# Optimization experiments

Hardware: AMD Instinct MI355X
Metric: run time of the kernel (lower is better)

## Reference

```python
import jax, jax.numpy as jnp
import numpy as np


def _conv1x1(x, w):
    # x [N,I,D,H,W], w [O,I]
    return jnp.einsum('nidhw,oi->nodhw', x, w)


def _conv3x3(x, w):
    return jax.lax.conv_general_dilated(
        x, w, window_strides=(1, 1, 1), padding=[(1, 1)] * 3,
        dimension_numbers=('NCDHW', 'OIDHW', 'NCDHW'))


def _interp_axis(x, out_len, axis):
    # linear interpolation along one axis, align_corners=True
    in_len = x.shape[axis]
    scale = (in_len - 1) / (out_len - 1)
    pos = jnp.arange(out_len, dtype=x.dtype) * scale
    lo = jnp.clip(jnp.floor(pos).astype(jnp.int32), 0, in_len - 1)
    hi = jnp.minimum(lo + 1, in_len - 1)
    frac = pos - lo.astype(x.dtype)
    shp = [1] * x.ndim
    shp[axis] = out_len
    frac = frac.reshape(shp)
    return jnp.take(x, lo, axis=axis) * (1 - frac) + jnp.take(x, hi, axis=axis) * frac


def _upsample_trilinear_ac(x, size):
    for ax, s in zip((2, 3, 4), size):
        x = _interp_axis(x, s, ax)
    return x


def _grid_sample_3d(inp, grid):
    # inp [N,C,D,H,W]; grid [N,Do,Ho,Wo,3] with channels (x=w, y=h, z=d) in [-1,1]
    # matches torch grid_sample defaults: trilinear, align_corners=False, zeros padding
    N, C, D, H, W = inp.shape
    ix = ((grid[..., 0] + 1) * W - 1) * 0.5
    iy = ((grid[..., 1] + 1) * H - 1) * 0.5
    iz = ((grid[..., 2] + 1) * D - 1) * 0.5
    x0 = jnp.floor(ix).astype(jnp.int32)
    y0 = jnp.floor(iy).astype(jnp.int32)
    z0 = jnp.floor(iz).astype(jnp.int32)
    fx = ix - x0.astype(inp.dtype)
    fy = iy - y0.astype(inp.dtype)
    fz = iz - z0.astype(inp.dtype)
    flat = inp.reshape(N, C, D * H * W)
    out = jnp.zeros((N, C) + grid.shape[1:4], dtype=inp.dtype)
    for dz, wz in ((0, 1 - fz), (1, fz)):
        for dy, wy in ((0, 1 - fy), (1, fy)):
            for dx, wx in ((0, 1 - fx), (1, fx)):
                zc = z0 + dz
                yc = y0 + dy
                xc = x0 + dx
                valid = (zc >= 0) & (zc < D) & (yc >= 0) & (yc < H) & (xc >= 0) & (xc < W)
                idx = (jnp.clip(zc, 0, D - 1) * H + jnp.clip(yc, 0, H - 1)) * W + jnp.clip(xc, 0, W - 1)
                vals = jax.vmap(lambda f, i: f[:, i])(flat, idx)  # [N,C,Do,Ho,Wo]
                w = (wz * wy * wx) * valid.astype(inp.dtype)
                out = out + vals * w[:, None]
    return out


def _point_reinforce(x, w_atten, w_conv):
    # SE-style: global avg pool -> 1x1 conv -> sigmoid -> residual scale -> 1x1 conv
    pooled = jnp.mean(x, axis=(2, 3, 4), keepdims=True)
    atten = jax.nn.sigmoid(_conv1x1(pooled, w_atten))
    x = x + x * atten
    return _conv1x1(x, w_conv)


def _forward(x, y, w_down_h, w_down_l, w_flow, w_att_atten, w_att_conv):
    D, H, W = x.shape[2:]
    low = _conv1x1(x, w_down_l)
    low = _point_reinforce(low, w_att_atten, w_att_conv)
    hf = _conv1x1(y, w_down_h)
    hf = _upsample_trilinear_ac(hf, (D, H, W))
    flow = _conv3x3(jnp.concatenate([hf, low], axis=1), w_flow)  # [N,3,D,H,W]
    # coordinate grid, channel order (w, h, d) as in the original flow_warp
    gw = jnp.broadcast_to(jnp.arange(W, dtype=x.dtype)[None, None, :], (D, H, W))
    gh = jnp.broadcast_to(jnp.arange(H, dtype=x.dtype)[None, :, None], (D, H, W))
    gd = jnp.broadcast_to(jnp.arange(D, dtype=x.dtype)[:, None, None], (D, H, W))
    grid = jnp.stack([gw, gh, gd], axis=0)[None]  # [1,3,D,H,W]
    norm = jnp.array([W, H, D], dtype=x.dtype)
    # NOTE: faithful to original -- divides by size only (grid ends up in [0,1), not [-1,1])
    vgrid = jnp.transpose(grid + flow, (0, 2, 3, 4, 1)) / norm  # [N,D,H,W,3]
    return _grid_sample_3d(y, vgrid)


def setup_inputs() -> dict:
    key = jax.random.key(0)
    ks = jax.random.split(key, 7)
    inplane_l, inplane_h, outplane = 64, 128, 64
    x = jax.random.normal(ks[0], (2, inplane_l, 16, 64, 64), dtype=jnp.float32)
    y = jax.random.normal(ks[1], (2, inplane_h, 8, 32, 32), dtype=jnp.float32)
    s = 0.05
    w_down_h = jax.random.normal(ks[2], (outplane, inplane_h), dtype=jnp.float32) * s
    w_down_l = jax.random.normal(ks[3], (outplane, inplane_l), dtype=jnp.float32) * s
    w_flow = jax.random.normal(ks[4], (3, 2 * outplane, 3, 3, 3), dtype=jnp.float32) * s
    w_att_atten = jax.random.normal(ks[5], (inplane_l, inplane_l), dtype=jnp.float32) * s
    w_att_conv = jax.random.normal(ks[6], (inplane_l, inplane_l), dtype=jnp.float32) * s
    return {'x': x, 'y': y, 'w_down_h': w_down_h, 'w_down_l': w_down_l,
            'w_flow': w_flow, 'w_att_atten': w_att_atten, 'w_att_conv': w_att_conv}


def reference(x, y, w_down_h, w_down_l, w_flow, w_att_atten, w_att_conv):
    return _forward(x, y, w_down_h, w_down_l, w_flow, w_att_atten, w_att_conv)
```

## Files before the change

### kernel.cpp

```cpp
#include <hip/hip_runtime.h>
#include <math.h>


#define MEANX_OFF  0
#define WEFF_OFF   128
#define HF_OFF     16384
#define HFUP_OFF   1064960
#define VG_OFF     9453568
#define ZPAGE_OFF  9846784

__global__ __launch_bounds__(256) void kearly(const float* __restrict__ x,
                                              const float* __restrict__ y,
                                              const float* __restrict__ wdh,
                                              float* __restrict__ meanx,
                                              float* __restrict__ hf,
                                              float* __restrict__ zpage) {
    const int blk = blockIdx.x;
    if (blk < 128) {
        if (blk == 0 && threadIdx.x < 64) zpage[threadIdx.x] = 0.f;
        int ch = blk;
        const float4* base = (const float4*)(x + (size_t)ch * 65536);
        float s = 0.f;
        for (int j = threadIdx.x; j < 16384; j += 256) {
            float4 v = base[j];
            s += v.x + v.y + v.z + v.w;
        }
        __shared__ float red[256];
        red[threadIdx.x] = s;
        __syncthreads();
        for (int off = 128; off > 0; off >>= 1) {
            if (threadIdx.x < off) red[threadIdx.x] += red[threadIdx.x + off];
            __syncthreads();
        }
        if (threadIdx.x == 0) meanx[ch] = red[0] * (1.0f / 65536.0f);
    } else {
        const int b = blk - 128;
        const int n = b >> 7;
        const int r = b & 127;
        const int os = r & 3;
        const int tile = r >> 2;
        const int p = tile * 256 + threadIdx.x;
        const float* yb = y + (size_t)n * 128 * 8192 + p;

        float acc[16];
#pragma unroll
        for (int o = 0; o < 16; ++o) acc[o] = 0.f;

        for (int i = 0; i < 128; i += 4) {
            const float yi0 = yb[(size_t)(i + 0) * 8192];
            const float yi1 = yb[(size_t)(i + 1) * 8192];
            const float yi2 = yb[(size_t)(i + 2) * 8192];
            const float yi3 = yb[(size_t)(i + 3) * 8192];
#pragma unroll
            for (int o = 0; o < 16; ++o) {
                float a = acc[o];
                a = fmaf(wdh[(os * 16 + o) * 128 + i + 0], yi0, a);
                a = fmaf(wdh[(os * 16 + o) * 128 + i + 1], yi1, a);
                a = fmaf(wdh[(os * 16 + o) * 128 + i + 2], yi2, a);
                a = fmaf(wdh[(os * 16 + o) * 128 + i + 3], yi3, a);
                acc[o] = a;
            }
        }
        float* ob = hf + (size_t)(n * 64 + os * 16) * 8192 + p;
#pragma unroll
        for (int o = 0; o < 16; ++o)
            ob[(size_t)o * 8192] = acc[o];
    }
}

__global__ __launch_bounds__(256) void kprep(const float* __restrict__ wdl,
                                             const float* __restrict__ watt,
                                             const float* __restrict__ wconv,
                                             const float* __restrict__ wflow,
                                             const float* __restrict__ meanx,
                                             float* __restrict__ weff) {
    const int n = blockIdx.x;
    const int tid = threadIdx.x;
    __shared__ float s_wdl[4096];
    __shared__ float s_wcT[4096];
    __shared__ float s_flow[5184];
    __shared__ float pooled[64], sc[64];
    for (int k = tid; k < 4096; k += 256) {
        s_wdl[k] = wdl[k];
        int o = k >> 6, j = k & 63;
        s_wcT[j * 64 + o] = wconv[k];
    }
    for (int k = tid; k < 5184; k += 256) {
        int o = k / 1728, r = k - o * 1728;
        s_flow[k] = wflow[o * 3456 + 1728 + r];
    }
    __syncthreads();
    if (tid < 64) {
        float p = 0.f;
        for (int i = 0; i < 64; ++i) p += s_wdl[tid * 64 + i] * meanx[n * 64 + i];
        pooled[tid] = p;
    }
    __syncthreads();
    if (tid < 64) {
        float a = 0.f;
        for (int i = 0; i < 64; ++i) a += watt[tid * 64 + i] * pooled[i];
        sc[tid] = 1.f + 1.f / (1.f + expf(-a));
    }
    __syncthreads();
    float wc[16];
#pragma unroll
    for (int k = 0; k < 16; ++k) {
        const int idx = tid + 256 * k;
        const int o = idx & 63, i = idx >> 6;
        float acc = 0.f;
#pragma unroll 8
        for (int j = 0; j < 64; ++j)
            acc += s_wcT[j * 64 + o] * (sc[j] * s_wdl[j * 64 + i]);
        wc[k] = acc;
    }
    __syncthreads();
#pragma unroll
    for (int k = 0; k < 16; ++k) {
        const int idx = tid + 256 * k;
        const int o = idx & 63, i = idx >> 6;
        s_wdl[i * 64 + o] = wc[k];
    }
    __syncthreads();
    for (int e = tid; e < 5184; e += 256) {
        const int i = e / 81, r = e - i * 81;
        const int o = r / 27, tap = r - o * 27;
        float acc = 0.f;
#pragma unroll 8
        for (int c = 0; c < 64; ++c)
            acc += s_flow[o * 1728 + c * 27 + tap] * s_wdl[i * 64 + c];
        weff[n * 5184 + e] = acc;
    }
}

__global__ __launch_bounds__(256) void kmid(const float* __restrict__ x,
                                            const float* __restrict__ ws,
                                            const float* __restrict__ weff,
                                            const float* __restrict__ hf,
                                            float* __restrict__ hfup,
                                            float* __restrict__ part) {
    const int blk = blockIdx.x;
    if (blk < 1024) {
        const int tid = threadIdx.x;
        const int sp = blk & 7;
        const int tile = blk >> 3;
        const int n = tile >> 6;
        const int t = tile & 63;
        const int td = t >> 4, th = (t >> 2) & 3, tw = t & 3;
        const int d0 = td * 4, h0 = th * 16, w0 = tw * 16;
        const int xo = tid & 3, ty = (tid >> 2) & 15, tz = tid >> 6;
        const int wv = tid >> 6;

        __shared__ float lds[3][2048];

        const float* gb = x + (size_t)(n * 64 + sp * 8) * 65536;
        const float* zp = ws + ZPAGE_OFF;

        const float* addrk[8];
        int vmask = 0;
#pragma unroll
        for (int k = 0; k < 8; ++k) {
            const int e = tid + 256 * k;
            const int r = e / 18;
            const int lx = e - r * 18;
            const int z = r / 18;
            const int ly = r - z * 18;
            const int gz = d0 - 1 + z, gy = h0 - 1 + ly, gx = w0 - 1 + lx;
            const bool ok = (e < 1944) && ((unsigned)gz < 16u) && ((unsigned)gy < 64u) &&
                            ((unsigned)gx < 64u);
            addrk[k] = ok ? (gb + (gz * 4096 + gy * 64 + gx)) : zp;
            vmask |= (ok ? 1 : 0) << k;
        }

#define STAGEL(BUFI)                                                                  \
    {                                                                                 \
        _Pragma("unroll")                                                             \
        for (int k = 0; k < 8; ++k) {                                                 \
            __builtin_amdgcn_global_load_lds(                                         \
                (const __attribute__((address_space(1))) unsigned int*)(addrk[k]),    \
                (__attribute__((address_space(3))) unsigned int*)                     \
                    (&lds[BUFI][wv * 64 + 256 * k]),                                  \
                4, 0, 0);                                                             \
            addrk[k] += ((vmask >> k) & 1) ? 65536 : 0;                               \
        }                                                                             \
    }

        float acc[3][4];
#pragma unroll
        for (int o = 0; o < 3; ++o)
#pragma unroll
            for (int j = 0; j < 4; ++j) acc[o][j] = 0.f;

        STAGEL(0);

        for (int ci = 0; ci < 8; ++ci) {
            const int cur = ci % 3;
            if (ci < 7) {
                STAGEL((ci + 1) % 3);
                asm volatile("s_waitcnt vmcnt(8)" ::: "memory");
            } else {
                asm volatile("s_waitcnt vmcnt(0)" ::: "memory");
            }
            __builtin_amdgcn_s_barrier();
            __builtin_amdgcn_sched_barrier(0);

            const int cidx = __builtin_amdgcn_readfirstlane(sp * 8 + ci);
            const float* wbase = weff + (size_t)n * 5184 + (size_t)cidx * 81;
            const float* buf = lds[cur];
#pragma unroll
            for (int dz = 0; dz < 3; ++dz) {
#pragma unroll
                for (int dy = 0; dy < 3; ++dy) {
                    const float* rp = &buf[((tz + dz) * 18 + ty + dy) * 18 + 4 * xo];
                    const float2 a0 = *(const float2*)(rp);
                    const float2 a1 = *(const float2*)(rp + 2);
                    const float2 a2 = *(const float2*)(rp + 4);
                    const float v[6] = {a0.x, a0.y, a1.x, a1.y, a2.x, a2.y};
                    float wq[3][3];
#pragma unroll
                    for (int o = 0; o < 3; ++o)
#pragma unroll
                        for (int dx = 0; dx < 3; ++dx)
                            wq[o][dx] = wbase[o * 27 + (dz * 3 + dy) * 3 + dx];
#pragma unroll
                    for (int o = 0; o < 3; ++o)
#pragma unroll
                        for (int j = 0; j < 4; ++j)
#pragma unroll
                            for (int dx = 0; dx < 3; ++dx)
                                acc[o][j] = fmaf(wq[o][dx], v[j + dx], acc[o][j]);
                }
            }
        }
#undef STAGEL

        const int oz = d0 + tz, oy = h0 + ty, ox = w0 + 4 * xo;
        const size_t base = ((size_t)((sp + 8) * 2 + n)) * 3 * 65536;
        const int p = oz * 4096 + oy * 64 + ox;
#pragma unroll
        for (int o = 0; o < 3; ++o)
            *(float4*)(part + base + (size_t)o * 65536 + p) =
                make_float4(acc[o][0], acc[o][1], acc[o][2], acc[o][3]);
    } else {
        int id2 = (blk - 1024) * 256 + threadIdx.x;
        int wp = id2 & 31, h = (id2 >> 5) & 63, d = (id2 >> 11) & 15;
        int c = (id2 >> 15) & 63, n = id2 >> 21;
        const float SD = 7.0f / 15.0f, SH = 31.0f / 63.0f;
        float pd = (float)d * SD, ph = (float)h * SH;
        int z0 = (int)pd; if (z0 > 7) z0 = 7;
        int z1 = min(z0 + 1, 7); float fz = pd - (float)z0;
        int y0 = (int)ph; if (y0 > 31) y0 = 31;
        int y1 = min(y0 + 1, 31); float fy = ph - (float)y0;

        const int w0i = 2 * wp, w1i = 2 * wp + 1;
        float pw0 = (float)w0i * SH, pw1 = (float)w1i * SH;
        int xa = (int)pw0; if (xa > 31) xa = 31;
        float fx0 = pw0 - (float)xa;
        int xb2 = (int)pw1; if (xb2 > 31) xb2 = 31;
        float fx1 = pw1 - (float)xb2;

        const float* b = hf + (size_t)(n * 64 + c) * 8192;
        const int r00 = (z0 * 32 + y0) * 32, r01 = (z0 * 32 + y1) * 32;
        const int r10 = (z1 * 32 + y0) * 32, r11 = (z1 * 32 + y1) * 32;
        const float wzy00 = (1.f - fz) * (1.f - fy), wzy01 = (1.f - fz) * fy;
        const float wzy10 = fz * (1.f - fy), wzy11 = fz * fy;

        float colv[3];
#pragma unroll
        for (int j = 0; j < 3; ++j) {
            int xc = min(xa + j, 31);
            colv[j] = wzy00 * b[r00 + xc] + wzy01 * b[r01 + xc] +
                      wzy10 * b[r10 + xc] + wzy11 * b[r11 + xc];
        }
        float o0 = colv[0] + (colv[1] - colv[0]) * fx0;
        int i1 = xb2 - xa;
        float lo = (i1 == 0) ? colv[0] : colv[1];
        float hi = (i1 == 0) ? colv[1] : colv[2];
        float o1 = lo + (hi - lo) * fx1;

        *(float2*)(hfup + ((size_t)id2 * 2)) = make_float2(o0, o1);
    }
}

__global__ __launch_bounds__(256) void kflowp(const float* __restrict__ ws,
                                              const float* __restrict__ wflow,
                                              float* __restrict__ part) {
    const int tid = threadIdx.x;
    const int b = blockIdx.x;
    const int split = b & 7;
    const int tile = b >> 3;
    const int n = tile >> 6;
    const int t = tile & 63;
    const int td = t >> 4, th = (t >> 2) & 3, tw = t & 3;
    const int d0 = td * 4, h0 = th * 16, w0 = tw * 16;
    const int xo = tid & 3, ty = (tid >> 2) & 15, tz = tid >> 6;
    const int wv = tid >> 6;

    __shared__ float lds[3][2048];

    const int srcb = HFUP_OFF + (n * 64 + split * 8) * 65536;

    int woff[8];
#pragma unroll
    for (int k = 0; k < 8; ++k) {
        const int e = tid + 256 * k;
        const int r = e / 18;
        const int lx = e - r * 18;
        const int z = r / 18;
        const int ly = r - z * 18;
        const int gz = d0 - 1 + z, gy = h0 - 1 + ly, gx = w0 - 1 + lx;
        const bool ok = (e < 1944) && ((unsigned)gz < 16u) && ((unsigned)gy < 64u) &&
                        ((unsigned)gx < 64u);
        woff[k] = ok ? (srcb + gz * 4096 + gy * 64 + gx) : ZPAGE_OFF;
    }

#define STAGE(BUFI, CI)                                                               \
    {                                                                                 \
        _Pragma("unroll")                                                             \
        for (int k = 0; k < 8; ++k) {                                                 \
            const int off = woff[k] + ((woff[k] < ZPAGE_OFF) ? (CI) * 65536 : 0);     \
            __builtin_amdgcn_global_load_lds(                                         \
                (const __attribute__((address_space(1))) unsigned int*)(ws + off),    \
                (__attribute__((address_space(3))) unsigned int*)                     \
                    (&lds[BUFI][wv * 64 + 256 * k]),                                  \
                4, 0, 0);                                                             \
        }                                                                             \
    }

    float acc[3][4];
#pragma unroll
    for (int o = 0; o < 3; ++o)
#pragma unroll
        for (int j = 0; j < 4; ++j) acc[o][j] = 0.f;

    STAGE(0, 0);

    for (int ci = 0; ci < 8; ++ci) {
        const int cur = ci % 3;
        if (ci < 7) {
            STAGE((ci + 1) % 3, ci + 1);
            asm volatile("s_waitcnt vmcnt(8)" ::: "memory");
        } else {
            asm volatile("s_waitcnt vmcnt(0)" ::: "memory");
        }
        __builtin_amdgcn_s_barrier();
        __builtin_amdgcn_sched_barrier(0);

        const int cgs = __builtin_amdgcn_readfirstlane(split * 8 + ci);
        const float* wb = wflow + (size_t)cgs * 27;
        const float* buf = lds[cur];
#pragma unroll
        for (int dz = 0; dz < 3; ++dz) {
#pragma unroll
            for (int dy = 0; dy < 3; ++dy) {
                const float* rp = &buf[((tz + dz) * 18 + ty + dy) * 18 + 4 * xo];
                const float2 a0 = *(const float2*)(rp);
                const float2 a1 = *(const float2*)(rp + 2);
                const float2 a2 = *(const float2*)(rp + 4);
                const float v[6] = {a0.x, a0.y, a1.x, a1.y, a2.x, a2.y};
                float wq[3][3];
#pragma unroll
                for (int o = 0; o < 3; ++o)
#pragma unroll
                    for (int dx = 0; dx < 3; ++dx)
                        wq[o][dx] = wb[o * 3456 + (dz * 3 + dy) * 3 + dx];
#pragma unroll
                for (int o = 0; o < 3; ++o)
#pragma unroll
                    for (int j = 0; j < 4; ++j)
#pragma unroll
                        for (int dx = 0; dx < 3; ++dx)
                            acc[o][j] = fmaf(wq[o][dx], v[j + dx], acc[o][j]);
            }
        }
    }
#undef STAGE

    const int oz = d0 + tz, oy = h0 + ty, ox = w0 + 4 * xo;
    const size_t base = ((size_t)(split * 2 + n)) * 3 * 65536;
    const int p = oz * 4096 + oy * 64 + ox;
#pragma unroll
    for (int o = 0; o < 3; ++o)
        *(float4*)(part + base + (size_t)o * 65536 + p) =
            make_float4(acc[o][0], acc[o][1], acc[o][2], acc[o][3]);
}

__global__ __launch_bounds__(256) void kpost(const float* __restrict__ part,
                                             const float* __restrict__ y,
                                             float* __restrict__ vg,
                                             float* __restrict__ yt) {
    const int blk = blockIdx.x;
    if (blk < 128) {
        int gid = blk * 256 + threadIdx.x;
        int n = gid >> 14, p4 = (gid & 16383) * 4;
        float4 s0 = make_float4(0.f, 0.f, 0.f, 0.f);
        float4 s1 = s0, s2 = s0;
        for (int s = 0; s < 16; ++s) {
            const float* bp = part + ((size_t)(s * 2 + n)) * 3 * 65536 + p4;
            float4 a = *(const float4*)(bp);
            float4 b4 = *(const float4*)(bp + 65536);
            float4 c4 = *(const float4*)(bp + 131072);
            s0.x += a.x; s0.y += a.y; s0.z += a.z; s0.w += a.w;
            s1.x += b4.x; s1.y += b4.y; s1.z += b4.z; s1.w += b4.w;
            s2.x += c4.x; s2.y += c4.y; s2.z += c4.z; s2.w += c4.w;
        }
        int w = p4 & 63, h = (p4 >> 6) & 63, d = p4 >> 12;
        size_t vb = (size_t)n * 3 * 65536;
        *(float4*)(vg + vb + p4) = make_float4(
            ((float)(w + 0) + s0.x) * (1.0f / 64.0f), ((float)(w + 1) + s0.y) * (1.0f / 64.0f),
            ((float)(w + 2) + s0.z) * (1.0f / 64.0f), ((float)(w + 3) + s0.w) * (1.0f / 64.0f));
        *(float4*)(vg + vb + 65536 + p4) = make_float4(
            ((float)h + s1.x) * (1.0f / 64.0f), ((float)h + s1.y) * (1.0f / 64.0f),
            ((float)h + s1.z) * (1.0f / 64.0f), ((float)h + s1.w) * (1.0f / 64.0f));
        *(float4*)(vg + vb + 131072 + p4) = make_float4(
            ((float)d + s2.x) * (1.0f / 16.0f), ((float)d + s2.y) * (1.0f / 16.0f),
            ((float)d + s2.z) * (1.0f / 16.0f), ((float)d + s2.w) * (1.0f / 16.0f));
    } else {
        int b = blk - 128;
        int n = b >> 8;
        int rem = b & 255;
        int ct = rem >> 7, st = rem & 127;
        int c0 = ct * 64, s0 = st * 64;
        __shared__ float t[64][65];
        int tx = threadIdx.x & 63, ty = threadIdx.x >> 6;
#pragma unroll
        for (int k = 0; k < 16; ++k)
            t[ty + 4 * k][tx] = y[((size_t)(n * 128 + c0 + ty + 4 * k)) * 8192 + s0 + tx];
        __syncthreads();
#pragma unroll
        for (int k = 0; k < 16; ++k)
            yt[((size_t)(n * 8192 + s0 + ty + 4 * k)) * 128 + c0 + tx] = t[tx][ty + 4 * k];
    }
}

__global__ __launch_bounds__(256) void ksample(const float* __restrict__ yt,
                                               const float* __restrict__ vg,
                                               float* __restrict__ out) {
    const int b = blockIdx.x;
    const int n = b >> 10;
    const int p0 = (b & 1023) << 6;
    const int tid = threadIdx.x;
    const int lane = tid & 63;
    const int wv = tid >> 6;

    __shared__ float lds[128 * 65];
    __shared__ float s_w[8][64];
    __shared__ int   s_idx[8][64];

    const float* ytn = yt + (size_t)n * 8192 * 128;
    const size_t vb = (size_t)n * 3 * 65536;

    if (tid < 64) {
        const int p = p0 + tid;
        float gx = vg[vb + p], gy = vg[vb + 65536 + p], gz = vg[vb + 131072 + p];
        float ix = ((gx + 1.f) * 32.f - 1.f) * 0.5f;
        float iy = ((gy + 1.f) * 32.f - 1.f) * 0.5f;
        float iz = ((gz + 1.f) * 8.f - 1.f) * 0.5f;
        int x0 = (int)floorf(ix), y0 = (int)floorf(iy), z0 = (int)floorf(iz);
        float fx = ix - (float)x0, fy = iy - (float)y0, fz = iz - (float)z0;
        float wx[2] = {1.f - fx, fx}, wy[2] = {1.f - fy, fy}, wz[2] = {1.f - fz, fz};
#pragma unroll
        for (int k = 0; k < 8; ++k) {
            int dz = k >> 2, dy = (k >> 1) & 1, dx = k & 1;
            int zc = z0 + dz, yc = y0 + dy, xc = x0 + dx;
            bool valid = ((unsigned)zc < 8u) && ((unsigned)yc < 32u) && ((unsigned)xc < 32u);
            int zcl = min(max(zc, 0), 7), ycl = min(max(yc, 0), 31), xcl = min(max(xc, 0), 31);
            s_idx[k][tid] = (zcl * 32 + ycl) * 32 + xcl;
            float wgt = wz[dz] * wy[dy] * wx[dx];
            s_w[k][tid] = valid ? wgt : 0.f;
        }
    }
    __syncthreads();

    for (int q = 0; q < 16; ++q) {
        const int pt = wv * 16 + q;
        float ax = 0.f, ay = 0.f;
#pragma unroll
        for (int k = 0; k < 8; ++k) {
            const float wk = s_w[k][pt];
            const int ik = s_idx[k][pt];
            const float2 v = *(const float2*)(ytn + (size_t)ik * 128 + 2 * lane);
            ax = fmaf(wk, v.x, ax);
            ay = fmaf(wk, v.y, ay);
        }
        lds[(2 * lane) * 65 + pt] = ax;
        lds[(2 * lane + 1) * 65 + pt] = ay;
    }
    __syncthreads();
    const int pw = tid & 63, cw = tid >> 6;
    float* ob = out + (size_t)n * 128 * 65536 + p0 + pw;
#pragma unroll
    for (int k = 0; k < 32; ++k) {
        int c = k * 4 + cw;
        ob[(size_t)c * 65536] = lds[c * 65 + pw];
    }
}

extern "C" void kernel_launch(void* const* d_in, const int* in_sizes, int n_in,
                              void* d_out, int out_size, void* d_ws, size_t ws_size,
                              hipStream_t stream) {
    const float* x     = (const float*)d_in[0];
    const float* y     = (const float*)d_in[1];
    const float* wdh   = (const float*)d_in[2];
    const float* wdl   = (const float*)d_in[3];
    const float* wflow = (const float*)d_in[4];
    const float* watt  = (const float*)d_in[5];
    const float* wconv = (const float*)d_in[6];
    float* out = (float*)d_out;

    float* ws     = (float*)d_ws;
    float* meanx  = ws + MEANX_OFF;
    float* weff   = ws + WEFF_OFF;
    float* hf     = ws + HF_OFF;
    float* hfup   = ws + HFUP_OFF;
    float* vg     = ws + VG_OFF;
    float* zpage  = ws + ZPAGE_OFF;

    float* part = out;
    float* yt = hfup;

    kearly<<<384, 256, 0, stream>>>(x, y, wdh, meanx, hf, zpage);
    kprep<<<2, 256, 0, stream>>>(wdl, watt, wconv, wflow, meanx, weff);
    kmid<<<17408, 256, 0, stream>>>(x, ws, weff, hf, hfup, part);
    kflowp<<<1024, 256, 0, stream>>>(ws, wflow, part);
    kpost<<<640, 256, 0, stream>>>(part, y, vg, yt);
    ksample<<<2048, 256, 0, stream>>>(yt, vg, out);
}
```

Before: 165.9 us.

## Remove kpost by moving y transpose into kearly and split-sum into ksample

The separate post-processing kernel is removed. The y transpose now runs as extra blocks of the first kernel, and the 16-way split-K reduction of flow partials plus grid construction moves into the sampling kernel's prologue. Partials and the transposed y now get their own workspace regions instead of aliasing the output and hfup. This saves one launch and the vg write/read round trip, at the cost of extra per-block reduction latency in ksample and more workspace memory.

```diff
diff --git a/kernel.cpp b/kernel.cpp
--- a/kernel.cpp
+++ b/kernel.cpp
@@ -6,14 +6,16 @@
 #define WEFF_OFF   128
 #define HF_OFF     16384
 #define HFUP_OFF   1064960
-#define VG_OFF     9453568
-#define ZPAGE_OFF  9846784
+#define ZPAGE_OFF  9453568
+#define YT_OFF     9453632
+#define PART_OFF   11550784
 
 __global__ __launch_bounds__(256) void kearly(const float* __restrict__ x,
                                               const float* __restrict__ y,
                                               const float* __restrict__ wdh,
                                               float* __restrict__ meanx,
                                               float* __restrict__ hf,
+                                              float* __restrict__ yt,
                                               float* __restrict__ zpage) {
     const int blk = blockIdx.x;
     if (blk < 128) {
@@ -33,7 +35,7 @@
             __syncthreads();
         }
         if (threadIdx.x == 0) meanx[ch] = red[0] * (1.0f / 65536.0f);
-    } else {
+    } else if (blk < 384) {
         const int b = blk - 128;
         const int n = b >> 7;
         const int r = b & 127;
@@ -65,6 +67,21 @@
 #pragma unroll
         for (int o = 0; o < 16; ++o)
             ob[(size_t)o * 8192] = acc[o];
+    } else {
+        int b = blk - 384;
+        int n = b >> 8;
+        int rem = b & 255;
+        int ct = rem >> 7, st = rem & 127;
+        int c0 = ct * 64, s0 = st * 64;
+        __shared__ float t[64][65];
+        int tx = threadIdx.x & 63, ty = threadIdx.x >> 6;
+#pragma unroll
+        for (int k = 0; k < 16; ++k)
+            t[ty + 4 * k][tx] = y[((size_t)(n * 128 + c0 + ty + 4 * k)) * 8192 + s0 + tx];
+        __syncthreads();
+#pragma unroll
+        for (int k = 0; k < 16; ++k)
+            yt[((size_t)(n * 8192 + s0 + ty + 4 * k)) * 128 + c0 + tx] = t[tx][ty + 4 * k];
     }
 }
 
@@ -384,56 +401,8 @@
             make_float4(acc[o][0], acc[o][1], acc[o][2], acc[o][3]);
 }
 
-__global__ __launch_bounds__(256) void kpost(const float* __restrict__ part,
-                                             const float* __restrict__ y,
-                                             float* __restrict__ vg,
-                                             float* __restrict__ yt) {
-    const int blk = blockIdx.x;
-    if (blk < 128) {
-        int gid = blk * 256 + threadIdx.x;
-        int n = gid >> 14, p4 = (gid & 16383) * 4;
-        float4 s0 = make_float4(0.f, 0.f, 0.f, 0.f);
-        float4 s1 = s0, s2 = s0;
-        for (int s = 0; s < 16; ++s) {
-            const float* bp = part + ((size_t)(s * 2 + n)) * 3 * 65536 + p4;
-            float4 a = *(const float4*)(bp);
-            float4 b4 = *(const float4*)(bp + 65536);
-            float4 c4 = *(const float4*)(bp + 131072);
-            s0.x += a.x; s0.y += a.y; s0.z += a.z; s0.w += a.w;
-            s1.x += b4.x; s1.y += b4.y; s1.z += b4.z; s1.w += b4.w;
-            s2.x += c4.x; s2.y += c4.y; s2.z += c4.z; s2.w += c4.w;
-        }
-        int w = p4 & 63, h = (p4 >> 6) & 63, d = p4 >> 12;
-        size_t vb = (size_t)n * 3 * 65536;
-        *(float4*)(vg + vb + p4) = make_float4(
-            ((float)(w + 0) + s0.x) * (1.0f / 64.0f), ((float)(w + 1) + s0.y) * (1.0f / 64.0f),
-            ((float)(w + 2) + s0.z) * (1.0f / 64.0f), ((float)(w + 3) + s0.w) * (1.0f / 64.0f));
-        *(float4*)(vg + vb + 65536 + p4) = make_float4(
-            ((float)h + s1.x) * (1.0f / 64.0f), ((float)h + s1.y) * (1.0f / 64.0f),
-            ((float)h + s1.z) * (1.0f / 64.0f), ((float)h + s1.w) * (1.0f / 64.0f));
-        *(float4*)(vg + vb + 131072 + p4) = make_float4(
-            ((float)d + s2.x) * (1.0f / 16.0f), ((float)d + s2.y) * (1.0f / 16.0f),
-            ((float)d + s2.z) * (1.0f / 16.0f), ((float)d + s2.w) * (1.0f / 16.0f));
-    } else {
-        int b = blk - 128;
-        int n = b >> 8;
-        int rem = b & 255;
-        int ct = rem >> 7, st = rem & 127;
-        int c0 = ct * 64, s0 = st * 64;
-        __shared__ float t[64][65];
-        int tx = threadIdx.x & 63, ty = threadIdx.x >> 6;
-#pragma unroll
-        for (int k = 0; k < 16; ++k)
-            t[ty + 4 * k][tx] = y[((size_t)(n * 128 + c0 + ty + 4 * k)) * 8192 + s0 + tx];
-        __syncthreads();
-#pragma unroll
-        for (int k = 0; k < 16; ++k)
-            yt[((size_t)(n * 8192 + s0 + ty + 4 * k)) * 128 + c0 + tx] = t[tx][ty + 4 * k];
-    }
-}
-
 __global__ __launch_bounds__(256) void ksample(const float* __restrict__ yt,
-                                               const float* __restrict__ vg,
+                                               const float* __restrict__ part,
                                                float* __restrict__ out) {
     const int b = blockIdx.x;
     const int n = b >> 10;
@@ -443,15 +412,29 @@
     const int wv = tid >> 6;
 
     __shared__ float lds[128 * 65];
+    __shared__ float s_sum[3][64];
     __shared__ float s_w[8][64];
     __shared__ int   s_idx[8][64];
 
     const float* ytn = yt + (size_t)n * 8192 * 128;
-    const size_t vb = (size_t)n * 3 * 65536;
+
+    if (tid < 192) {
+        const int o = tid >> 6, pt = tid & 63;
+        const int p = p0 + pt;
+        float s = 0.f;
+#pragma unroll
+        for (int sp = 0; sp < 16; ++sp)
+            s += part[((size_t)(sp * 2 + n) * 3 + o) * 65536 + p];
+        s_sum[o][pt] = s;
+    }
+    __syncthreads();
 
     if (tid < 64) {
         const int p = p0 + tid;
-        float gx = vg[vb + p], gy = vg[vb + 65536 + p], gz = vg[vb + 131072 + p];
+        const int w = p & 63, h = (p >> 6) & 63, d = p >> 12;
+        float gx = ((float)w + s_sum[0][tid]) * (1.0f / 64.0f);
+        float gy = ((float)h + s_sum[1][tid]) * (1.0f / 64.0f);
+        float gz = ((float)d + s_sum[2][tid]) * (1.0f / 16.0f);
         float ix = ((gx + 1.f) * 32.f - 1.f) * 0.5f;
         float iy = ((gy + 1.f) * 32.f - 1.f) * 0.5f;
         float iz = ((gz + 1.f) * 8.f - 1.f) * 0.5f;
@@ -512,16 +495,13 @@
     float* weff   = ws + WEFF_OFF;
     float* hf     = ws + HF_OFF;
     float* hfup   = ws + HFUP_OFF;
-    float* vg     = ws + VG_OFF;
     float* zpage  = ws + ZPAGE_OFF;
-
-    float* part = out;
-    float* yt = hfup;
-
-    kearly<<<384, 256, 0, stream>>>(x, y, wdh, meanx, hf, zpage);
+    float* yt     = ws + YT_OFF;
+    float* part   = ws + PART_OFF;
+
+    kearly<<<896, 256, 0, stream>>>(x, y, wdh, meanx, hf, yt, zpage);
     kprep<<<2, 256, 0, stream>>>(wdl, watt, wconv, wflow, meanx, weff);
     kmid<<<17408, 256, 0, stream>>>(x, ws, weff, hf, hfup, part);
     kflowp<<<1024, 256, 0, stream>>>(ws, wflow, part);
-    kpost<<<640, 256, 0, stream>>>(part, y, vg, yt);
-    ksample<<<2048, 256, 0, stream>>>(yt, vg, out);
+    ksample<<<2048, 256, 0, stream>>>(yt, part, out);
 }
```

Measured after the change: 158.7 us. -4.3%, faster.
